# Kernel tuning notes

Measured on AMD Instinct MI355X. Metric: run time of the kernel, lower is better.

The kernel has to match this reference:

```python
import jax, jax.numpy as jnp
import numpy as np

V, C, D, L, H = 32000, 1024, 1024, 12, 16
HD = D // H


def setup_inputs() -> dict:
    key = jax.random.key(0)
    ks = jax.random.split(key, 20)
    B, T = 2, 1024
    s = 0.02
    inp = {
        "context": jax.random.randint(ks[0], (B, T), 0, V),
        "tok_emb": jax.random.normal(ks[1], (V, D), jnp.float32) * s,
        "pos_emb": jax.random.normal(ks[2], (C, D), jnp.float32) * s,
        # per-layer stacked params (weights stored [in, out])
        "wq": jax.random.normal(ks[3], (L, D, D), jnp.float32) * s,
        "wk": jax.random.normal(ks[4], (L, D, D), jnp.float32) * s,
        "wv": jax.random.normal(ks[5], (L, D, D), jnp.float32) * s,
        "ln1_s": jnp.ones((L, D), jnp.float32),
        "ln1_b": jnp.zeros((L, D), jnp.float32),
        "ln2_s": jnp.ones((L, D), jnp.float32),
        "ln2_b": jnp.zeros((L, D), jnp.float32),
        "fw1": jax.random.normal(ks[6], (L, D, D), jnp.float32) * s,
        "fb1": jnp.zeros((L, D), jnp.float32),
        "fw2": jax.random.normal(ks[7], (L, D, D), jnp.float32) * s,
        "fb2": jnp.zeros((L, D), jnp.float32),
        "lnf_s": jnp.ones((D,), jnp.float32),
        "lnf_b": jnp.zeros((D,), jnp.float32),
        "wp": jax.random.normal(ks[8], (D, V), jnp.float32) * s,
        "bp": jnp.zeros((V,), jnp.float32),
    }
    return inp


def _ln(x, scale, bias, eps=1e-5):
    m = jnp.mean(x, axis=-1, keepdims=True)
    v = jnp.mean(jnp.square(x - m), axis=-1, keepdims=True)
    return (x - m) * jax.lax.rsqrt(v + eps) * scale + bias


def reference(context, tok_emb, pos_emb, wq, wk, wv, ln1_s, ln1_b, ln2_s, ln2_b,
              fw1, fb1, fw2, fb2, lnf_s, lnf_b, wp, bp):
    B, T = context.shape
    x = tok_emb[context] + pos_emb[:T]  # [B,T,D]
    causal = jnp.tril(jnp.ones((T, T), bool))

    def block(x, p):
        (wq_, wk_, wv_, s1, b1, s2, b2, w1_, b1f, w2_, b2f) = p
        h = _ln(x, s1, b1)
        # concatenated per-head projections == full [D,D] matmul + head reshape
        q = (h @ wq_).reshape(B, T, H, HD)
        k = (h @ wk_).reshape(B, T, H, HD)
        v = (h @ wv_).reshape(B, T, H, HD)
        scores = jnp.einsum('bthd,bshd->bhts', q, k) / np.sqrt(HD)
        scores = jnp.where(causal, scores, -jnp.inf)
        attn = jax.nn.softmax(scores, axis=-1)
        o = jnp.einsum('bhts,bshd->bthd', attn, v).reshape(B, T, D)
        x = x + o
        h2 = _ln(x, s2, b2)
        f = jax.nn.relu(h2 @ w1_ + b1f) @ w2_ + b2f  # dropout in eval mode (identity)
        return x + f, None

    x, _ = jax.lax.scan(block, x, (wq, wk, wv, ln1_s, ln1_b, ln2_s, ln2_b, fw1, fb1, fw2, fb2))
    logits = _ln(x, lnf_s, lnf_b) @ wp + bp
    return jax.nn.softmax(logits, axis=-1)
```

## Files before the change

### kernel.cpp

```cpp
#include <hip/hip_runtime.h>
#include <hip/hip_bf16.h>

typedef unsigned short u16;
typedef float f32x4 __attribute__((ext_vector_type(4)));
typedef __bf16 bf16x8 __attribute__((ext_vector_type(8)));
typedef short s16x8 __attribute__((ext_vector_type(8)));


__device__ __forceinline__ u16 f2b(float f) {
  union { __hip_bfloat16 h; u16 u; } c;
  c.h = __float2bfloat16(f);
  return c.u;
}

__device__ __forceinline__ void gload16(const void* g, void* l) {
  __builtin_amdgcn_global_load_lds(
      (const __attribute__((address_space(1))) unsigned int*)g,
      (__attribute__((address_space(3))) unsigned int*)l, 16, 0, 0);
}

__device__ __forceinline__ float block_sum(float v, float* sred) {
  const int tid = threadIdx.x;
#pragma unroll
  for (int off = 32; off >= 1; off >>= 1) v += __shfl_down(v, off);
  if ((tid & 63) == 0) sred[tid >> 6] = v;
  __syncthreads();
  float r = sred[0] + sred[1] + sred[2] + sred[3];
  __syncthreads();
  return r;
}

__device__ __forceinline__ f32x4 fmax4(f32x4 a, f32x4 b) {
  f32x4 r;
  r[0] = fmaxf(a[0], b[0]); r[1] = fmaxf(a[1], b[1]);
  r[2] = fmaxf(a[2], b[2]); r[3] = fmaxf(a[3], b[3]);
  return r;
}


template<int ROWS>
__device__ __forceinline__ void stage_tile(const u16* g, int ld, char* ldsb, int tid) {
#pragma unroll
  for (int i = 0; i < ROWS / 64; ++i) {
    int c = i * 256 + tid;
    int row = c >> 2;
    int k8 = (c & 3) ^ ((row >> 1) & 3);
    gload16(g + (size_t)row * ld + k8 * 8, ldsb + i * 4096 + (tid & 192) * 16);
  }
}

template<int MI, int NI, int WCN>
__device__ __forceinline__ void compute_tile(const char* lA, const char* lB, f32x4 (&acc)[MI][NI]) {
  const int tid = threadIdx.x;
  const int lane = tid & 63;
  const int w = tid >> 6;
  const int wr = w / WCN, wc = w % WCN;
  const int fr = lane & 15, k8 = lane >> 4;
  bf16x8 a[MI], b[NI];
#pragma unroll
  for (int mi = 0; mi < MI; ++mi) {
    int row = wr * (MI * 16) + mi * 16 + fr;
    a[mi] = *(const bf16x8*)(lA + row * 64 + ((k8 ^ ((row >> 1) & 3)) << 4));
  }
#pragma unroll
  for (int ni = 0; ni < NI; ++ni) {
    int row = wc * (NI * 16) + ni * 16 + fr;
    b[ni] = *(const bf16x8*)(lB + row * 64 + ((k8 ^ ((row >> 1) & 3)) << 4));
  }
#pragma unroll
  for (int mi = 0; mi < MI; ++mi)
#pragma unroll
    for (int ni = 0; ni < NI; ++ni)
      acc[mi][ni] = __builtin_amdgcn_mfma_f32_16x16x32_bf16(a[mi], b[ni], acc[mi][ni], 0, 0, 0);
}

template<int MI, int NI, int WRN, int WCN, int BMT, int BNT>
__device__ __forceinline__ void gemm_core(const u16* A, int lda, const u16* B, int ldb,
                                          int nkt, char* lds, f32x4 (&acc)[MI][NI]) {
  const int tid = threadIdx.x;
  const int bufSz = BMT * 64 + BNT * 64;
  stage_tile<BMT>(A, lda, lds, tid);
  stage_tile<BNT>(B, ldb, lds + BMT * 64, tid);
  __syncthreads();
  int cur = 0;
  for (int kt = 0; kt < nkt; ++kt) {
    if (kt + 1 < nkt) {
      char* nb = lds + (cur ^ 1) * bufSz;
      stage_tile<BMT>(A + (size_t)(kt + 1) * 32, lda, nb, tid);
      stage_tile<BNT>(B + (size_t)(kt + 1) * 32, ldb, nb + BMT * 64, tid);
    }
    char* cb = lds + cur * bufSz;
    compute_tile<MI, NI, WCN>(cb, cb + BMT * 64, acc);
    __syncthreads();
    cur ^= 1;
  }
}


template<int ROWS>
__device__ __forceinline__ void stage64(const u16* g, int ld, char* ldsb, int tid) {
#pragma unroll
  for (int i = 0; i < ROWS / 32; ++i) {
    int c = i * 256 + tid;
    int row = c >> 3;
    int slot = (c & 7) ^ (row & 7);
    gload16(g + (size_t)row * ld + slot * 8, ldsb + i * 4096 + (tid & 192) * 16);
  }
}

__device__ __forceinline__ bf16x8 ldread64(const char* base, int row, int slot) {
  return *(const bf16x8*)(base + row * 128 + ((slot ^ (row & 7)) << 4));
}


__global__ __launch_bounds__(256) void embed_kernel(const int* __restrict__ ctx,
    const float* __restrict__ tok, const float* __restrict__ pos, float* __restrict__ x) {
  const int row = blockIdx.x, tid = threadIdx.x;
  const int t = row & 1023;
  const int id = ctx[row];
  float4 a = ((const float4*)(tok + (size_t)id * 1024))[tid];
  float4 p = ((const float4*)(pos + (size_t)t * 1024))[tid];
  a.x += p.x; a.y += p.y; a.z += p.z; a.w += p.w;
  ((float4*)(x + (size_t)row * 1024))[tid] = a;
}

__global__ __launch_bounds__(256) void layernorm_bf16(const float* __restrict__ x,
    const float* __restrict__ sc, const float* __restrict__ bi, u16* __restrict__ h) {
  __shared__ float sred[4];
  const int row = blockIdx.x, tid = threadIdx.x;
  const float4 v = ((const float4*)(x + (size_t)row * 1024))[tid];
  float mean = block_sum(v.x + v.y + v.z + v.w, sred) * (1.f / 1024.f);
  const float dx = v.x - mean, dy = v.y - mean, dz = v.z - mean, dw = v.w - mean;
  float var = block_sum(dx * dx + dy * dy + dz * dz + dw * dw, sred) * (1.f / 1024.f);
  const float rs = rsqrtf(var + 1e-5f);
  const float4 s4 = ((const float4*)sc)[tid];
  const float4 b4 = ((const float4*)bi)[tid];
  ushort4 o;
  o.x = f2b(dx * rs * s4.x + b4.x);
  o.y = f2b(dy * rs * s4.y + b4.y);
  o.z = f2b(dz * rs * s4.z + b4.z);
  o.w = f2b(dw * rs * s4.w + b4.w);
  ((ushort4*)(h + (size_t)row * 1024))[tid] = o;
}

__device__ __forceinline__ void transpose_body(const float* __restrict__ src,
                                               u16* __restrict__ dst, int N) {
  __shared__ float tile[32][33];
  const int tid = threadIdx.x;
  const int tx = tid & 31, ty = tid >> 5;
  const int kt = blockIdx.y * 32, nt = blockIdx.x * 32;
#pragma unroll
  for (int i = 0; i < 4; ++i) {
    int r = ty + i * 8;
    tile[r][tx] = src[(size_t)(kt + r) * N + nt + tx];
  }
  __syncthreads();
#pragma unroll
  for (int i = 0; i < 4; ++i) {
    int r = ty + i * 8;
    dst[(size_t)(nt + r) * 1024 + kt + tx] = f2b(tile[tx][r]);
  }
}

__global__ __launch_bounds__(256) void transpose_cvt(const float* __restrict__ src,
    u16* __restrict__ dst, int N, size_t srcStride, size_t dstStride) {
  transpose_body(src + blockIdx.z * srcStride, dst + blockIdx.z * dstStride, N);
}

__global__ __launch_bounds__(256) void transpose_qkv(const float* __restrict__ wq,
    const float* __restrict__ wk, const float* __restrict__ wv, u16* __restrict__ dst) {
  const int z = blockIdx.z, l = z / 3, which = z - l * 3;
  const float* src = (which == 0 ? wq : (which == 1 ? wk : wv)) + (size_t)l * 1048576;
  u16* d = dst + (size_t)l * 3145728 + (size_t)which * 1048576;
  transpose_body(src, d, 1024);
}

template<int MI, int NI, int WRN, int WCN, bool BIAS, bool RELU, bool RESID, bool OUTBF,
         bool XSWAP, int SWIZ>
__global__ __launch_bounds__(256) void gemm_bt(const u16* __restrict__ A, int lda,
    const u16* __restrict__ Bt, int ldb, const float* __restrict__ bias,
    const float* __restrict__ resid, void* __restrict__ out, int ldc, int nkt) {
  constexpr int BMT = WRN * MI * 16;
  constexpr int BNT = WCN * NI * 16;
  __shared__ __align__(128) char lds[2 * (BMT * 64 + BNT * 64)];
  int bmi, bni;
  if (SWIZ > 0) {
    const int v = blockIdx.x;
    const int vp = (v & 7) * SWIZ + (v >> 3);
    bni = vp >> 4;
    bmi = vp & 15;
  } else {
    bmi = XSWAP ? blockIdx.x : blockIdx.y;
    bni = XSWAP ? blockIdx.y : blockIdx.x;
  }
  const size_t bm = (size_t)bmi * BMT, bn = (size_t)bni * BNT;
  const f32x4 vz = {0.f, 0.f, 0.f, 0.f};
  f32x4 acc[MI][NI];
#pragma unroll
  for (int i = 0; i < MI; ++i)
#pragma unroll
    for (int j = 0; j < NI; ++j) acc[i][j] = vz;
  gemm_core<MI, NI, WRN, WCN, BMT, BNT>(A + bm * lda, lda, Bt + bn * ldb, ldb, nkt, lds, acc);
  const int tid = threadIdx.x, lane = tid & 63, w = tid >> 6;
  const int wr = w / WCN, wc = w % WCN, fr = lane & 15, k8 = lane >> 4;
#pragma unroll
  for (int mi = 0; mi < MI; ++mi)
#pragma unroll
    for (int ni = 0; ni < NI; ++ni) {
      const size_t c = bn + wc * (NI * 16) + ni * 16 + fr;
      const float bv = BIAS ? bias[c] : 0.f;
#pragma unroll
      for (int j = 0; j < 4; ++j) {
        const size_t r = bm + wr * (MI * 16) + mi * 16 + k8 * 4 + j;
        float v = acc[mi][ni][j] + bv;
        if (RELU) v = fmaxf(v, 0.f);
        if (RESID) v += resid[r * (size_t)ldc + c];
        if (OUTBF) ((u16*)out)[r * (size_t)ldc + c] = f2b(v);
        else       ((float*)out)[r * (size_t)ldc + c] = v;
      }
    }
}

__global__ __launch_bounds__(256) void gather_vT(const u16* __restrict__ qkv,
    u16* __restrict__ vT) {
  const int st = blockIdx.x;
  const int bh = blockIdx.y;
  const int b = bh >> 4, h = bh & 15;
  __shared__ u16 tile[64][80];
  const int tid = threadIdx.x;
#pragma unroll
  for (int i = 0; i < 2; ++i) {
    int c = i * 256 + tid;
    int sl = c >> 3, h8 = c & 7;
    *(s16x8*)&tile[sl][h8 * 8] =
        *(const s16x8*)(qkv + (size_t)(b * 1024 + st * 64 + sl) * 3072 + 2048 + h * 64 + h8 * 8);
  }
  __syncthreads();
#pragma unroll
  for (int i = 0; i < 2; ++i) {
    int c = i * 256 + tid;
    int hd = c >> 3, s8 = c & 7;
    s16x8 o;
#pragma unroll
    for (int j = 0; j < 8; ++j) o[j] = (short)tile[s8 * 8 + j][hd];
    *(s16x8*)(vT + ((size_t)bh * 64 + hd) * 1024 + st * 64 + s8 * 8) = o;
  }
}

__global__ __launch_bounds__(256) void attn_flash(const u16* __restrict__ qkv,
    const u16* __restrict__ vT, float* __restrict__ x) {
  const int bh = blockIdx.x;
  const int qt = blockIdx.y;
  const int b = bh >> 4, h = bh & 15;
  __shared__ __align__(128) char lds[40960];
  char* Qs = lds;
  char* Ks = lds + 8192;
  char* Vs = lds + 24576;
  const int tid = threadIdx.x, lane = tid & 63, w = tid >> 6;
  const int fr = lane & 15, k8 = lane >> 4;
  char* Pw = Qs + w * 2048;
  const u16* qbase = qkv + (size_t)(b * 1024 + qt * 64) * 3072 + h * 64;
  const u16* kbase = qkv + (size_t)(b * 1024) * 3072 + 1024 + h * 64;
  const u16* vbase = vT + (size_t)bh * 65536;

  stage64<64>(qbase, 3072, Qs, tid);
  stage64<64>(kbase, 3072, Ks, tid);
  stage64<64>(vbase, 1024, Vs, tid);
  __syncthreads();

  bf16x8 aq[2];
#pragma unroll
  for (int kk = 0; kk < 2; ++kk)
    aq[kk] = ldread64(Qs, w * 16 + fr, kk * 4 + k8);

  const f32x4 vz = {0.f, 0.f, 0.f, 0.f};
  f32x4 oacc[4];
  f32x4 m_ = {-1e30f, -1e30f, -1e30f, -1e30f};
  f32x4 l_ = vz;
#pragma unroll
  for (int ni = 0; ni < 4; ++ni) oacc[ni] = vz;

  const int nst = qt + 1;
  const int t0 = qt * 64 + w * 16;
  int cur = 0;
  for (int st = 0; st < nst; ++st) {
    if (st + 1 < nst) {
      stage64<64>(kbase + (size_t)(st + 1) * 64 * 3072, 3072, Ks + (cur ^ 1) * 8192, tid);
      stage64<64>(vbase + (st + 1) * 64, 1024, Vs + (cur ^ 1) * 8192, tid);
    }
    const char* Kc = Ks + cur * 8192;
    const char* Vc = Vs + cur * 8192;
    f32x4 sacc[4];
#pragma unroll
    for (int ni = 0; ni < 4; ++ni) sacc[ni] = vz;
#pragma unroll
    for (int kk = 0; kk < 2; ++kk) {
      bf16x8 bk[4];
#pragma unroll
      for (int ni = 0; ni < 4; ++ni) bk[ni] = ldread64(Kc, ni * 16 + fr, kk * 4 + k8);
#pragma unroll
      for (int ni = 0; ni < 4; ++ni)
        sacc[ni] = __builtin_amdgcn_mfma_f32_16x16x32_bf16(aq[kk], bk[ni], sacc[ni], 0, 0, 0);
    }
    const int sbase = st * 64;
    const bool needMask = (st == qt);
#pragma unroll
    for (int ni = 0; ni < 4; ++ni) {
      sacc[ni] *= 0.125f;
      if (needMask) {
        const int s = sbase + ni * 16 + fr;
#pragma unroll
        for (int j = 0; j < 4; ++j) {
          const int t = t0 + k8 * 4 + j;
          if (s > t) sacc[ni][j] = -1e30f;
        }
      }
    }
    f32x4 pm = fmax4(fmax4(sacc[0], sacc[1]), fmax4(sacc[2], sacc[3]));
#pragma unroll
    for (int msk = 1; msk <= 8; msk <<= 1) {
#pragma unroll
      for (int j = 0; j < 4; ++j) pm[j] = fmaxf(pm[j], __shfl_xor(pm[j], msk));
    }
    const f32x4 mn = fmax4(m_, pm);
    f32x4 alpha, rs = vz;
#pragma unroll
    for (int j = 0; j < 4; ++j) alpha[j] = __expf(m_[j] - mn[j]);
#pragma unroll
    for (int ni = 0; ni < 4; ++ni) {
#pragma unroll
      for (int j = 0; j < 4; ++j) {
        const float p = __expf(sacc[ni][j] - mn[j]);
        rs[j] += p;
        const int t_loc = k8 * 4 + j;
        const int s_loc = ni * 16 + fr;
        *(u16*)(Pw + t_loc * 128 + (((s_loc >> 3) ^ (t_loc & 7)) << 4) + (s_loc & 7) * 2) = f2b(p);
      }
    }
#pragma unroll
    for (int msk = 1; msk <= 8; msk <<= 1) {
#pragma unroll
      for (int j = 0; j < 4; ++j) rs[j] += __shfl_xor(rs[j], msk);
    }
    m_ = mn;
#pragma unroll
    for (int j = 0; j < 4; ++j) l_[j] = l_[j] * alpha[j] + rs[j];
#pragma unroll
    for (int ni = 0; ni < 4; ++ni) oacc[ni] *= alpha;
#pragma unroll
    for (int kk = 0; kk < 2; ++kk) {
      bf16x8 ap = ldread64(Pw, fr, kk * 4 + k8);
      bf16x8 bv[4];
#pragma unroll
      for (int ni = 0; ni < 4; ++ni) bv[ni] = ldread64(Vc, ni * 16 + fr, kk * 4 + k8);
#pragma unroll
      for (int ni = 0; ni < 4; ++ni)
        oacc[ni] = __builtin_amdgcn_mfma_f32_16x16x32_bf16(ap, bv[ni], oacc[ni], 0, 0, 0);
    }
    __syncthreads();
    cur ^= 1;
  }
  f32x4 invl;
#pragma unroll
  for (int j = 0; j < 4; ++j) invl[j] = 1.f / l_[j];
#pragma unroll
  for (int ni = 0; ni < 4; ++ni) {
    const int hd = ni * 16 + fr;
#pragma unroll
    for (int j = 0; j < 4; ++j) {
      const int t = t0 + k8 * 4 + j;
      x[(size_t)(b * 1024 + t) * 1024 + h * 64 + hd] += oacc[ni][j] * invl[j];
    }
  }
}

__global__ __launch_bounds__(256) void softmax_v(float* __restrict__ logits) {
  const int row = blockIdx.x, tid = threadIdx.x;
  float* lr = logits + (size_t)row * 32000;
  const float4* lr4 = (const float4*)lr;
  float mx = -1e30f, sm = 0.f;
  for (int i = tid; i < 8000; i += 256) {
    const float4 v = lr4[i];
    float vm = fmaxf(fmaxf(v.x, v.y), fmaxf(v.z, v.w));
    float m2 = fmaxf(mx, vm);
    sm = sm * __expf(mx - m2) + __expf(v.x - m2) + __expf(v.y - m2) +
         __expf(v.z - m2) + __expf(v.w - m2);
    mx = m2;
  }
  __shared__ float smx[4], ssm[4];
#pragma unroll
  for (int off = 32; off >= 1; off >>= 1) {
    float om = __shfl_down(mx, off), os = __shfl_down(sm, off);
    float m2 = fmaxf(mx, om);
    sm = sm * __expf(mx - m2) + os * __expf(om - m2);
    mx = m2;
  }
  if ((tid & 63) == 0) { smx[tid >> 6] = mx; ssm[tid >> 6] = sm; }
  __syncthreads();
  const float M = fmaxf(fmaxf(smx[0], smx[1]), fmaxf(smx[2], smx[3]));
  const float S = ssm[0] * __expf(smx[0] - M) + ssm[1] * __expf(smx[1] - M) +
                  ssm[2] * __expf(smx[2] - M) + ssm[3] * __expf(smx[3] - M);
  const float inv = 1.f / S;
  float4* lw4 = (float4*)lr;
  for (int i = tid; i < 8000; i += 256) {
    float4 v = lw4[i];
    v.x = __expf(v.x - M) * inv; v.y = __expf(v.y - M) * inv;
    v.z = __expf(v.z - M) * inv; v.w = __expf(v.w - M) * inv;
    lw4[i] = v;
  }
}


extern "C" void kernel_launch(void* const* d_in, const int* in_sizes, int n_in,
                              void* d_out, int out_size, void* d_ws, size_t ws_size,
                              hipStream_t stream) {
  const int*   ctx   = (const int*)d_in[0];
  const float* tok   = (const float*)d_in[1];
  const float* pos   = (const float*)d_in[2];
  const float* wq    = (const float*)d_in[3];
  const float* wk    = (const float*)d_in[4];
  const float* wv    = (const float*)d_in[5];
  const float* ln1_s = (const float*)d_in[6];
  const float* ln1_b = (const float*)d_in[7];
  const float* ln2_s = (const float*)d_in[8];
  const float* ln2_b = (const float*)d_in[9];
  const float* fw1   = (const float*)d_in[10];
  const float* fb1   = (const float*)d_in[11];
  const float* fw2   = (const float*)d_in[12];
  const float* fb2   = (const float*)d_in[13];
  const float* lnf_s = (const float*)d_in[14];
  const float* lnf_b = (const float*)d_in[15];
  const float* wp    = (const float*)d_in[16];
  const float* bp    = (const float*)d_in[17];
  float* out = (float*)d_out;

  char* ws = (char*)d_ws;
  size_t o = 0;
  auto get = [&](size_t bytes) {
    char* r = ws + o;
    o += (bytes + 255) & ~(size_t)255;
    return r;
  };
  u16*   wqkvT = (u16*)get(12ULL * 3072 * 1024 * 2);
  u16*   wf1T  = (u16*)get(12ULL * 1024 * 1024 * 2);
  u16*   wf2T  = (u16*)get(12ULL * 1024 * 1024 * 2);
  u16*   wpT   = (u16*)get(32000ULL * 1024 * 2);
  float* x     = (float*)get(2048ULL * 1024 * 4);
  u16*   h     = (u16*)get(2048ULL * 1024 * 2);
  u16*   qkvb  = (u16*)get(2048ULL * 3072 * 2);
  u16*   vT    = (u16*)get(32ULL * 64 * 1024 * 2);
  u16*   f1b   = (u16*)get(2048ULL * 1024 * 2);

  embed_kernel<<<2048, 256, 0, stream>>>(ctx, tok, pos, x);
  transpose_qkv<<<dim3(32, 32, 36), 256, 0, stream>>>(wq, wk, wv, wqkvT);
  transpose_cvt<<<dim3(32, 32, 12), 256, 0, stream>>>(fw1, wf1T, 1024, 1048576, 1048576);
  transpose_cvt<<<dim3(32, 32, 12), 256, 0, stream>>>(fw2, wf2T, 1024, 1048576, 1048576);
  transpose_cvt<<<dim3(1000, 32, 1), 256, 0, stream>>>(wp, wpT, 32000, 0, 0);

  for (int l = 0; l < 12; ++l) {
    layernorm_bf16<<<2048, 256, 0, stream>>>(x, ln1_s + l * 1024, ln1_b + l * 1024, h);
    gemm_bt<4, 4, 2, 2, false, false, false, true, false, 0><<<dim3(24, 16), 256, 0, stream>>>(
        h, 1024, wqkvT + (size_t)l * 3145728, 1024, nullptr, nullptr, qkvb, 3072, 32);
    gather_vT<<<dim3(16, 32), 256, 0, stream>>>(qkvb, vT);
    attn_flash<<<dim3(32, 16), 256, 0, stream>>>(qkvb, vT, x);
    layernorm_bf16<<<2048, 256, 0, stream>>>(x, ln2_s + l * 1024, ln2_b + l * 1024, h);
    gemm_bt<4, 2, 2, 2, true, true, false, true, false, 0><<<dim3(16, 16), 256, 0, stream>>>(
        h, 1024, wf1T + (size_t)l * 1048576, 1024, fb1 + l * 1024, nullptr, f1b, 1024, 32);
    gemm_bt<4, 2, 2, 2, true, false, true, false, false, 0><<<dim3(16, 16), 256, 0, stream>>>(
        f1b, 1024, wf2T + (size_t)l * 1048576, 1024, fb2 + l * 1024, x, x, 1024, 32);
  }

  layernorm_bf16<<<2048, 256, 0, stream>>>(x, lnf_s, lnf_b, h);
  gemm_bt<4, 4, 2, 2, true, false, false, false, false, 500><<<dim3(4000), 256, 0, stream>>>(
      h, 1024, wpT, 1024, bp, nullptr, out, 32000, 32);
  softmax_v<<<2048, 256, 0, stream>>>(out);
}
```

Measured before the change: 2.198 ms.

## Fuse V transpose into QKV GEMM, bf16 logits, retile FFN and vocab GEMMs

Replaces the QKV GEMM plus the separate gather_vT kernel with a qkv_gemm whose epilogue writes the V columns straight into the transposed vT layout, removing a launch and a round trip through memory. The FFN GEMMs move to smaller M tiles with twice as many blocks, and the vocab GEMM uses 128x64 tiles and writes bf16 logits into workspace aliased over the no-longer-needed transposed QKV and FFN weights. The softmax then reads those bf16 logits once into registers and writes fp32 output, which halves logit write traffic. The cost is extra rounding of logits to bf16 before softmax, and the aliasing relies on the layer weights being dead by the time the vocab GEMM runs.

Result: faster. 2.080 ms (-5.4%).

```diff
diff --git a/kernel.cpp b/kernel.cpp
--- a/kernel.cpp
+++ b/kernel.cpp
@@ -11,6 +11,12 @@
   union { __hip_bfloat16 h; u16 u; } c;
   c.h = __float2bfloat16(f);
   return c.u;
+}
+
+__device__ __forceinline__ float b2f(u16 u) {
+  union { unsigned i; float f; } c;
+  c.i = (unsigned)u << 16;
+  return c.f;
 }
 
 __device__ __forceinline__ void gload16(const void* g, void* l) {
@@ -221,29 +227,47 @@
     }
 }
 
-__global__ __launch_bounds__(256) void gather_vT(const u16* __restrict__ qkv,
-    u16* __restrict__ vT) {
-  const int st = blockIdx.x;
-  const int bh = blockIdx.y;
-  const int b = bh >> 4, h = bh & 15;
-  __shared__ u16 tile[64][80];
-  const int tid = threadIdx.x;
-#pragma unroll
-  for (int i = 0; i < 2; ++i) {
-    int c = i * 256 + tid;
-    int sl = c >> 3, h8 = c & 7;
-    *(s16x8*)&tile[sl][h8 * 8] =
-        *(const s16x8*)(qkv + (size_t)(b * 1024 + st * 64 + sl) * 3072 + 2048 + h * 64 + h8 * 8);
-  }
-  __syncthreads();
-#pragma unroll
-  for (int i = 0; i < 2; ++i) {
-    int c = i * 256 + tid;
-    int hd = c >> 3, s8 = c & 7;
-    s16x8 o;
-#pragma unroll
-    for (int j = 0; j < 8; ++j) o[j] = (short)tile[s8 * 8 + j][hd];
-    *(s16x8*)(vT + ((size_t)bh * 64 + hd) * 1024 + st * 64 + s8 * 8) = o;
+__global__ __launch_bounds__(256) void qkv_gemm(const u16* __restrict__ A,
+    const u16* __restrict__ Bt, u16* __restrict__ qkvb, u16* __restrict__ vT) {
+  __shared__ __align__(128) char lds[2 * (128 * 64 + 64 * 64)];
+  const int bni = blockIdx.x, bmi = blockIdx.y;
+  const size_t bm = (size_t)bmi * 128, bn = (size_t)bni * 64;
+  const f32x4 vz = {0.f, 0.f, 0.f, 0.f};
+  f32x4 acc[4][2];
+#pragma unroll
+  for (int i = 0; i < 4; ++i)
+#pragma unroll
+    for (int j = 0; j < 2; ++j) acc[i][j] = vz;
+  gemm_core<4, 2, 2, 2, 128, 64>(A + bm * 1024, 1024, Bt + bn * 1024, 1024, 32, lds, acc);
+  const int tid = threadIdx.x, lane = tid & 63, w = tid >> 6;
+  const int wr = w >> 1, wc = w & 1, fr = lane & 15, k8 = lane >> 4;
+  if (bni < 32) {
+#pragma unroll
+    for (int mi = 0; mi < 4; ++mi)
+#pragma unroll
+      for (int ni = 0; ni < 2; ++ni) {
+        const size_t c = bn + wc * 32 + ni * 16 + fr;
+#pragma unroll
+        for (int j = 0; j < 4; ++j) {
+          const size_t r = bm + wr * 64 + mi * 16 + k8 * 4 + j;
+          qkvb[r * 3072 + c] = f2b(acc[mi][ni][j]);
+        }
+      }
+  } else {
+    const int h = bni - 32;
+    const int b = (int)(bm >> 10);
+#pragma unroll
+    for (int mi = 0; mi < 4; ++mi)
+#pragma unroll
+      for (int ni = 0; ni < 2; ++ni) {
+        const int hd = wc * 32 + ni * 16 + fr;
+        const size_t rowV = ((size_t)(b * 16 + h)) * 64 + hd;
+        const int s0 = (int)((bm & 1023) + wr * 64 + mi * 16 + k8 * 4);
+        ushort4 q;
+        q.x = f2b(acc[mi][ni][0]); q.y = f2b(acc[mi][ni][1]);
+        q.z = f2b(acc[mi][ni][2]); q.w = f2b(acc[mi][ni][3]);
+        *(ushort4*)(vT + rowV * 1024 + s0) = q;
+      }
   }
 }
 
@@ -374,39 +398,56 @@
   }
 }
 
-__global__ __launch_bounds__(256) void softmax_v(float* __restrict__ logits) {
+__global__ __launch_bounds__(256) void softmax_v2(const u16* __restrict__ lg,
+                                                  float* __restrict__ out) {
   const int row = blockIdx.x, tid = threadIdx.x;
-  float* lr = logits + (size_t)row * 32000;
-  const float4* lr4 = (const float4*)lr;
-  float mx = -1e30f, sm = 0.f;
-  for (int i = tid; i < 8000; i += 256) {
-    const float4 v = lr4[i];
-    float vm = fmaxf(fmaxf(v.x, v.y), fmaxf(v.z, v.w));
-    float m2 = fmaxf(mx, vm);
-    sm = sm * __expf(mx - m2) + __expf(v.x - m2) + __expf(v.y - m2) +
-         __expf(v.z - m2) + __expf(v.w - m2);
-    mx = m2;
-  }
-  __shared__ float smx[4], ssm[4];
-#pragma unroll
-  for (int off = 32; off >= 1; off >>= 1) {
-    float om = __shfl_down(mx, off), os = __shfl_down(sm, off);
-    float m2 = fmaxf(mx, om);
-    sm = sm * __expf(mx - m2) + os * __expf(om - m2);
-    mx = m2;
-  }
-  if ((tid & 63) == 0) { smx[tid >> 6] = mx; ssm[tid >> 6] = sm; }
+  const u16* lr = lg + (size_t)row * 32000;
+  float* orow = out + (size_t)row * 32000;
+  s16x8 buf[16];
+  float mx = -1e30f;
+#pragma unroll
+  for (int c = 0; c < 16; ++c) {
+    const int idx = tid + c * 256;
+    if (idx < 4000) {
+      buf[c] = *(const s16x8*)(lr + idx * 8);
+#pragma unroll
+      for (int j = 0; j < 8; ++j) mx = fmaxf(mx, b2f((u16)buf[c][j]));
+    }
+  }
+  __shared__ float smx[4], ssum[4];
+#pragma unroll
+  for (int off = 32; off >= 1; off >>= 1) mx = fmaxf(mx, __shfl_down(mx, off));
+  if ((tid & 63) == 0) smx[tid >> 6] = mx;
   __syncthreads();
   const float M = fmaxf(fmaxf(smx[0], smx[1]), fmaxf(smx[2], smx[3]));
-  const float S = ssm[0] * __expf(smx[0] - M) + ssm[1] * __expf(smx[1] - M) +
-                  ssm[2] * __expf(smx[2] - M) + ssm[3] * __expf(smx[3] - M);
+  __syncthreads();
+  float sm = 0.f;
+#pragma unroll
+  for (int c = 0; c < 16; ++c) {
+    const int idx = tid + c * 256;
+    if (idx < 4000) {
+#pragma unroll
+      for (int j = 0; j < 8; ++j) sm += __expf(b2f((u16)buf[c][j]) - M);
+    }
+  }
+  const float S = block_sum(sm, ssum);
   const float inv = 1.f / S;
-  float4* lw4 = (float4*)lr;
-  for (int i = tid; i < 8000; i += 256) {
-    float4 v = lw4[i];
-    v.x = __expf(v.x - M) * inv; v.y = __expf(v.y - M) * inv;
-    v.z = __expf(v.z - M) * inv; v.w = __expf(v.w - M) * inv;
-    lw4[i] = v;
+#pragma unroll
+  for (int c = 0; c < 16; ++c) {
+    const int idx = tid + c * 256;
+    if (idx < 4000) {
+      float4 o0, o1;
+      o0.x = __expf(b2f((u16)buf[c][0]) - M) * inv;
+      o0.y = __expf(b2f((u16)buf[c][1]) - M) * inv;
+      o0.z = __expf(b2f((u16)buf[c][2]) - M) * inv;
+      o0.w = __expf(b2f((u16)buf[c][3]) - M) * inv;
+      o1.x = __expf(b2f((u16)buf[c][4]) - M) * inv;
+      o1.y = __expf(b2f((u16)buf[c][5]) - M) * inv;
+      o1.z = __expf(b2f((u16)buf[c][6]) - M) * inv;
+      o1.w = __expf(b2f((u16)buf[c][7]) - M) * inv;
+      *(float4*)(orow + idx * 8) = o0;
+      *(float4*)(orow + idx * 8 + 4) = o1;
+    }
   }
 }
 
@@ -441,15 +482,17 @@
     o += (bytes + 255) & ~(size_t)255;
     return r;
   };
+  u16*   wpT   = (u16*)get(32000ULL * 1024 * 2);
+  size_t aliasOff = o;
   u16*   wqkvT = (u16*)get(12ULL * 3072 * 1024 * 2);
   u16*   wf1T  = (u16*)get(12ULL * 1024 * 1024 * 2);
   u16*   wf2T  = (u16*)get(12ULL * 1024 * 1024 * 2);
-  u16*   wpT   = (u16*)get(32000ULL * 1024 * 2);
   float* x     = (float*)get(2048ULL * 1024 * 4);
   u16*   h     = (u16*)get(2048ULL * 1024 * 2);
   u16*   qkvb  = (u16*)get(2048ULL * 3072 * 2);
   u16*   vT    = (u16*)get(32ULL * 64 * 1024 * 2);
   u16*   f1b   = (u16*)get(2048ULL * 1024 * 2);
+  u16*   logitsb = (u16*)(ws + aliasOff);
 
   embed_kernel<<<2048, 256, 0, stream>>>(ctx, tok, pos, x);
   transpose_qkv<<<dim3(32, 32, 36), 256, 0, stream>>>(wq, wk, wv, wqkvT);
@@ -459,19 +502,17 @@
 
   for (int l = 0; l < 12; ++l) {
     layernorm_bf16<<<2048, 256, 0, stream>>>(x, ln1_s + l * 1024, ln1_b + l * 1024, h);
-    gemm_bt<4, 4, 2, 2, false, false, false, true, false, 0><<<dim3(24, 16), 256, 0, stream>>>(
-        h, 1024, wqkvT + (size_t)l * 3145728, 1024, nullptr, nullptr, qkvb, 3072, 32);
-    gather_vT<<<dim3(16, 32), 256, 0, stream>>>(qkvb, vT);
+    qkv_gemm<<<dim3(48, 16), 256, 0, stream>>>(h, wqkvT + (size_t)l * 3145728, qkvb, vT);
     attn_flash<<<dim3(32, 16), 256, 0, stream>>>(qkvb, vT, x);
     layernorm_bf16<<<2048, 256, 0, stream>>>(x, ln2_s + l * 1024, ln2_b + l * 1024, h);
-    gemm_bt<4, 2, 2, 2, true, true, false, true, false, 0><<<dim3(16, 16), 256, 0, stream>>>(
+    gemm_bt<2, 2, 2, 2, true, true, false, true, false, 0><<<dim3(16, 32), 256, 0, stream>>>(
         h, 1024, wf1T + (size_t)l * 1048576, 1024, fb1 + l * 1024, nullptr, f1b, 1024, 32);
-    gemm_bt<4, 2, 2, 2, true, false, true, false, false, 0><<<dim3(16, 16), 256, 0, stream>>>(
+    gemm_bt<2, 2, 2, 2, true, false, true, false, false, 0><<<dim3(16, 32), 256, 0, stream>>>(
         f1b, 1024, wf2T + (size_t)l * 1048576, 1024, fb2 + l * 1024, x, x, 1024, 32);
   }
 
   layernorm_bf16<<<2048, 256, 0, stream>>>(x, lnf_s, lnf_b, h);
-  gemm_bt<4, 4, 2, 2, true, false, false, false, false, 500><<<dim3(4000), 256, 0, stream>>>(
-      h, 1024, wpT, 1024, bp, nullptr, out, 32000, 32);
-  softmax_v<<<2048, 256, 0, stream>>>(out);
-}
+  gemm_bt<4, 2, 2, 2, true, false, false, true, false, 1000><<<dim3(8000), 256, 0, stream>>>(
+      h, 1024, wpT, 1024, bp, nullptr, logitsb, 32000, 32);
+  softmax_v2<<<2048, 256, 0, stream>>>(logitsb, out);
+}
```
